# Performance work log

Hardware: AMD Instinct MI355X
Metric: run time of the kernel (lower is better)

Reference implementation:

```python
import jax, jax.numpy as jnp
import numpy as np

N = 65536          # number of macroscopic states (road cells)
Q = 512            # Q_mesoscale: velocity quadrature points
VMIN, VMAX = 0.0, 70.0
STOP = 1e-3        # stop_criterion used in forward()
MAX_ITER = 100


def setup_inputs() -> dict:
    key = jax.random.key(0)
    # macro velocities in the interior of [VMIN, VMAX] so Newton is well-conditioned
    macro_velocity = jax.random.uniform(key, (N, 1), dtype=jnp.float32,
                                        minval=5.0, maxval=65.0)
    xi = jnp.linspace(VMIN, VMAX, Q, dtype=jnp.float32)  # buffer self.xi
    return {"macro_velocity": macro_velocity, "xi": xi}


def _moments(lam, xi, xi2):
    # lam: [N,1], xi/xi2: [Q] -> E: [N,Q]
    E = jnp.exp(lam * xi[None, :])
    S0 = E.sum(axis=1, keepdims=True)
    S1 = (E * xi[None, :]).sum(axis=1, keepdims=True)
    S2 = (E * xi2[None, :]).sum(axis=1, keepdims=True)
    return S0, S1, S2


def _solve_lambda_mu(macro_velocity, xi):
    xi2 = xi * xi
    lam0 = jnp.zeros_like(macro_velocity)
    S0, S1, S2 = _moments(lam0, xi, xi2)
    gprime = (S0 * S2 - S1 * S1) / (S0 * S0)

    def cond(state):
        lam, S0, S1, S2, gp, c = state
        return (c < MAX_ITER) & (jnp.max(jnp.abs(gp)) > STOP)

    def body(state):
        lam, S0, S1, S2, gp, c = state
        lam1 = lam - (S1 / S0 - macro_velocity) / gp
        S0n, S1n, S2n = _moments(lam1, xi, xi2)
        gpn = (S0n * S2n - S1n * S1n) / (S0n * S0n)
        return (lam1, S0n, S1n, S2n, gpn, c + 1)

    lam, S0, _, _, _, _ = jax.lax.while_loop(
        cond, body, (lam0, S0, S1, S2, gprime, jnp.int32(0)))
    mu0 = -jnp.log(S0)
    return lam, mu0


def reference(macro_velocity, xi):
    lam, mu0 = _solve_lambda_mu(macro_velocity, xi)
    # f_eq = exp(mu0) * exp(lambda * xi)  -> [N, Q]
    return jnp.exp(mu0) * jnp.exp(lam * xi[None, :])
```

## Files before the change

### kernel.cpp

```cpp
#include <hip/hip_runtime.h>
#include <math.h>

#define N_CELLS 65536
#define Q_PTS   512


__device__ __forceinline__ void moments_mv(double lam, double* m, double* v) {
    const double DX = 70.0 / 511.0;
    const double L  = 512.0 * 70.0 / 511.0;
    const double C2 = L * L - DX * DX;
    const double C4 = L * L * L * L - DX * DX * DX * DX;
    if (fabs(lam) > 1e-6) {
        double gL = 1.0 / (-expm1(-lam * L));
        double gd = 1.0 / (-expm1(-lam * DX));
        *m = L * gL - DX * gd;
        *v = L * L * (gL - gL * gL) - DX * DX * (gd - gd * gd);
    } else {
        *m = 35.0 + lam * (C2 / 12.0) - lam * lam * lam * (C4 / 720.0);
        *v = C2 / 12.0 - lam * lam * (C4 / 240.0);
    }
}

__global__ void __launch_bounds__(256)
solve_kernel(const float* __restrict__ u_in, float2* __restrict__ lm) {
    int i = blockIdx.x * blockDim.x + threadIdx.x;
    if (i >= N_CELLS) return;
    double u = (double)u_in[i];
    double lam = 0.0;
    for (int it = 0; it < 64; ++it) {
        double m, v;
        moments_mv(lam, &m, &v);
        double dl = (m - u) / v;
        lam -= dl;
        lam = fmin(fmax(lam, -2.0), 2.0);
        if (fabs(dl) < 1e-13 * (1.0 + fabs(lam))) break;
    }
    const double DX = 70.0 / 511.0;
    const double L  = 512.0 * 70.0 / 511.0;
    double logS0;
    if (fabs(lam) > 1e-6) {
        logS0 = log(expm1(lam * L) / expm1(lam * DX));
    } else {
        const double V0 = (L * L - DX * DX) / 12.0;
        logS0 = log(512.0) + lam * 35.0 + 0.5 * lam * lam * V0;
    }
    lm[i] = make_float2((float)lam, (float)(-logS0));
}

__global__ void __launch_bounds__(256)
feq_kernel(const float4* __restrict__ xi4,
           const float2* __restrict__ lm,
           float4* __restrict__ out4) {
    int idx  = blockIdx.x * blockDim.x + threadIdx.x;
    int cell = idx >> 7;
    int k    = idx & 127;
    float2 p = lm[cell];
    float4 x = xi4[k];
    float4 r;
    r.x = __expf(fmaf(p.x, x.x, p.y));
    r.y = __expf(fmaf(p.x, x.y, p.y));
    r.z = __expf(fmaf(p.x, x.z, p.y));
    r.w = __expf(fmaf(p.x, x.w, p.y));
    out4[idx] = r;
}

extern "C" void kernel_launch(void* const* d_in, const int* in_sizes, int n_in,
                              void* d_out, int out_size, void* d_ws, size_t ws_size,
                              hipStream_t stream) {
    const float* macro_u = (const float*)d_in[0];
    const float* xi      = (const float*)d_in[1];
    float* out = (float*)d_out;
    float2* lm = (float2*)d_ws;

    solve_kernel<<<(N_CELLS + 255) / 256, 256, 0, stream>>>(macro_u, lm);

    int total4 = N_CELLS * Q_PTS / 4;
    feq_kernel<<<total4 / 256, 256, 0, stream>>>((const float4*)xi, lm, (float4*)out);
}
```

Before: 31.70 us.

## Fuse Newton solve into exponential writer kernel with float warm-start iterations

Merges the per-cell Newton solve and the f_eq write into one kernel. Each block's first 16 threads solve 16 cells, running 9 fixed float iterations from a linearized initial guess and then 3 double refinement steps. The results go through shared memory, so the workspace round trip and the second launch are gone. The cost is that most threads in each block sit idle at the barrier during the serial solve. The fixed iteration count also drops the convergence check, so accuracy now depends on Newton converging within those steps.

```diff
diff --git a/kernel.cpp b/kernel.cpp
--- a/kernel.cpp
+++ b/kernel.cpp
@@ -3,65 +3,86 @@
 
 #define N_CELLS 65536
 #define Q_PTS   512
+#define CPB     16
+#define F4C     128
 
 
-__device__ __forceinline__ void moments_mv(double lam, double* m, double* v) {
-    const double DX = 70.0 / 511.0;
-    const double L  = 512.0 * 70.0 / 511.0;
-    const double C2 = L * L - DX * DX;
-    const double C4 = L * L * L * L - DX * DX * DX * DX;
-    if (fabs(lam) > 1e-6) {
-        double gL = 1.0 / (-expm1(-lam * L));
-        double gd = 1.0 / (-expm1(-lam * DX));
-        *m = L * gL - DX * gd;
-        *v = L * L * (gL - gL * gL) - DX * DX * (gd - gd * gd);
-    } else {
-        *m = 35.0 + lam * (C2 / 12.0) - lam * lam * lam * (C4 / 720.0);
-        *v = C2 / 12.0 - lam * lam * (C4 / 240.0);
+__global__ void __launch_bounds__(256)
+fused_kernel(const float* __restrict__ u_in,
+             const float4* __restrict__ xi4,
+             float4* __restrict__ out4) {
+    __shared__ float2 lm_s[CPB];
+    const int t = threadIdx.x;
+    const int cell0 = blockIdx.x * CPB;
+
+    if (t < CPB) {
+        const double DX = 70.0 / 511.0;
+        const double L  = 512.0 * 70.0 / 511.0;
+        const double C2 = L * L - DX * DX;
+        const double C4 = L * L * L * L - DX * DX * DX * DX;
+        const double V0 = C2 / 12.0;
+        const float  DXf = (float)DX, Lf = (float)L, V0f = (float)V0;
+
+        const float u = u_in[cell0 + t];
+
+        float lam = (u - 35.0f) / V0f;
+        #pragma unroll
+        for (int it = 0; it < 9; ++it) {
+            float m, v;
+            if (fabsf(lam) > 1e-3f) {
+                float gL = -1.0f / expm1f(-lam * Lf);
+                float gd = -1.0f / expm1f(-lam * DXf);
+                m = Lf * gL - DXf * gd;
+                v = Lf * Lf * (gL - gL * gL) - DXf * DXf * (gd - gd * gd);
+            } else {
+                m = 35.0f + lam * V0f;
+                v = V0f;
+            }
+            lam -= (m - u) / v;
+            lam = fminf(fmaxf(lam, -2.0f), 2.0f);
+        }
+
+        double lamd = (double)lam;
+        const double ud = (double)u;
+        #pragma unroll
+        for (int it = 0; it < 3; ++it) {
+            double m, v;
+            if (fabs(lamd) > 1e-6) {
+                double gL = 1.0 / (-expm1(-lamd * L));
+                double gd = 1.0 / (-expm1(-lamd * DX));
+                m = L * gL - DX * gd;
+                v = L * L * (gL - gL * gL) - DX * DX * (gd - gd * gd);
+            } else {
+                m = 35.0 + lamd * (C2 / 12.0) - lamd * lamd * lamd * (C4 / 720.0);
+                v = C2 / 12.0 - lamd * lamd * (C4 / 240.0);
+            }
+            lamd -= (m - ud) / v;
+            lamd = fmin(fmax(lamd, -2.0), 2.0);
+        }
+
+        double logS0;
+        if (fabs(lamd) > 1e-6) {
+            logS0 = log(expm1(lamd * L) / expm1(lamd * DX));
+        } else {
+            logS0 = log(512.0) + lamd * 35.0 + 0.5 * lamd * lamd * V0;
+        }
+        lm_s[t] = make_float2((float)lamd, (float)(-logS0));
     }
-}
+    __syncthreads();
 
-__global__ void __launch_bounds__(256)
-solve_kernel(const float* __restrict__ u_in, float2* __restrict__ lm) {
-    int i = blockIdx.x * blockDim.x + threadIdx.x;
-    if (i >= N_CELLS) return;
-    double u = (double)u_in[i];
-    double lam = 0.0;
-    for (int it = 0; it < 64; ++it) {
-        double m, v;
-        moments_mv(lam, &m, &v);
-        double dl = (m - u) / v;
-        lam -= dl;
-        lam = fmin(fmax(lam, -2.0), 2.0);
-        if (fabs(dl) < 1e-13 * (1.0 + fabs(lam))) break;
+    const int base = blockIdx.x * (CPB * F4C);
+    #pragma unroll
+    for (int i = 0; i < (CPB * F4C) / 256; ++i) {
+        int idx = i * 256 + t;
+        float2 p = lm_s[idx >> 7];
+        float4 x = xi4[idx & 127];
+        float4 r;
+        r.x = __expf(fmaf(p.x, x.x, p.y));
+        r.y = __expf(fmaf(p.x, x.y, p.y));
+        r.z = __expf(fmaf(p.x, x.z, p.y));
+        r.w = __expf(fmaf(p.x, x.w, p.y));
+        out4[base + idx] = r;
     }
-    const double DX = 70.0 / 511.0;
-    const double L  = 512.0 * 70.0 / 511.0;
-    double logS0;
-    if (fabs(lam) > 1e-6) {
-        logS0 = log(expm1(lam * L) / expm1(lam * DX));
-    } else {
-        const double V0 = (L * L - DX * DX) / 12.0;
-        logS0 = log(512.0) + lam * 35.0 + 0.5 * lam * lam * V0;
-    }
-    lm[i] = make_float2((float)lam, (float)(-logS0));
-}
-
-__global__ void __launch_bounds__(256)
-feq_kernel(const float4* __restrict__ xi4,
-           const float2* __restrict__ lm,
-           float4* __restrict__ out4) {
-    int idx  = blockIdx.x * blockDim.x + threadIdx.x;
-    int cell = idx >> 7;
-    int k    = idx & 127;
-    float2 p = lm[cell];
-    float4 x = xi4[k];
-    float4 r;
-    r.x = __expf(fmaf(p.x, x.x, p.y));
-    r.y = __expf(fmaf(p.x, x.y, p.y));
-    r.z = __expf(fmaf(p.x, x.z, p.y));
-    r.w = __expf(fmaf(p.x, x.w, p.y));
-    out4[idx] = r;
 }
 
 extern "C" void kernel_launch(void* const* d_in, const int* in_sizes, int n_in,
@@ -70,10 +91,7 @@
     const float* macro_u = (const float*)d_in[0];
     const float* xi      = (const float*)d_in[1];
     float* out = (float*)d_out;
-    float2* lm = (float2*)d_ws;
 
-    solve_kernel<<<(N_CELLS + 255) / 256, 256, 0, stream>>>(macro_u, lm);
-
-    int total4 = N_CELLS * Q_PTS / 4;
-    feq_kernel<<<total4 / 256, 256, 0, stream>>>((const float4*)xi, lm, (float4*)out);
+    fused_kernel<<<N_CELLS / CPB, 256, 0, stream>>>(
+        macro_u, (const float4*)xi, (float4*)out);
 }
```

After: 29.65 us. 6.5% less time.
